# Performance work log

Hardware: AMD Instinct MI355X
Metric: run time of the kernel (lower is better)

The kernel has to match this reference:

```python
import jax, jax.numpy as jnp
import numpy as np


def _binarize(w):
    # adaptive per-output-channel scale: alpha = mean(|w|) over input dim (detached)
    alpha = jax.lax.stop_gradient(jnp.mean(jnp.abs(w), axis=1, keepdims=True))
    bw = alpha * jnp.sign(w)
    # straight-through estimator: forward uses bw, backward passes grad to w
    return w + jax.lax.stop_gradient(bw - w)


def setup_inputs() -> dict:
    key = jax.random.key(0)
    k1, k2, k3, k4, k5 = jax.random.split(key, 5)
    D, H = 1024, 4096
    x = jax.random.normal(k1, (64, 196, D), dtype=jnp.float32)
    w1 = jax.random.normal(k2, (H, D), dtype=jnp.float32) * 0.02
    b1 = jax.random.normal(k3, (H,), dtype=jnp.float32) * 0.02
    w2 = jax.random.normal(k4, (D, H), dtype=jnp.float32) * 0.02
    b2 = jax.random.normal(k5, (D,), dtype=jnp.float32) * 0.02
    return {"x": x, "w1": w1, "b1": b1, "w2": w2, "b2": b2}


def reference(x, w1, b1, w2, b2):
    # fc1: binary-weight linear -> GELU (exact, erf) -> fc2: binary-weight linear
    # dropout prob = 0.0 -> identity
    bw1 = _binarize(w1)  # [H, D]
    h = jnp.einsum('bsd,hd->bsh', x, bw1) + b1  # [B, S, H]
    h = jax.nn.gelu(h, approximate=False)
    bw2 = _binarize(w2)  # [D, H]
    out = jnp.einsum('bsh,dh->bsd', h, bw2) + b2  # [B, S, D]
    return out
```

## Files before the change

kernel.cpp:

```cpp
#include <hip/hip_runtime.h>
#include <hip/hip_bf16.h>
#include <cstdint>
#include <cstddef>

typedef __bf16 bf16x8 __attribute__((ext_vector_type(8)));
typedef float f32x4 __attribute__((ext_vector_type(4)));

#define AS1(p) ((const __attribute__((address_space(1))) void*)(p))
#define AS3(p) ((__attribute__((address_space(3))) void*)(p))
#define LDSA(p) ((unsigned)(size_t)(const __attribute__((address_space(3))) unsigned short*)(p))

__device__ __forceinline__ unsigned short f2bf_rne(float f) {
    union { float f; unsigned u; } c; c.f = f;
    unsigned u = c.u;
    unsigned r = (u + 0x7FFFu + ((u >> 16) & 1u)) >> 16;
    return (unsigned short)r;
}

__global__ __launch_bounds__(256)
void binarize_k(const float* __restrict__ W, unsigned short* __restrict__ Sg,
                float* __restrict__ Alpha, int C) {
    const int r = blockIdx.x;
    const float4* w = (const float4*)(W + (size_t)r * C);
    ushort4* s = (ushort4*)(Sg + (size_t)r * C);
    const int n4 = C >> 2;
    float lsum = 0.f;
    for (int i = threadIdx.x; i < n4; i += 256) {
        float4 v = w[i];
        lsum += fabsf(v.x) + fabsf(v.y) + fabsf(v.z) + fabsf(v.w);
        ushort4 o;
        o.x = (v.x == 0.f) ? 0 : ((v.x < 0.f) ? 0xBF80 : 0x3F80);
        o.y = (v.y == 0.f) ? 0 : ((v.y < 0.f) ? 0xBF80 : 0x3F80);
        o.z = (v.z == 0.f) ? 0 : ((v.z < 0.f) ? 0xBF80 : 0x3F80);
        o.w = (v.w == 0.f) ? 0 : ((v.w < 0.f) ? 0xBF80 : 0x3F80);
        s[i] = o;
    }
    for (int o = 32; o > 0; o >>= 1) lsum += __shfl_down(lsum, o, 64);
    __shared__ float red[4];
    const int lane = threadIdx.x & 63, wid = threadIdx.x >> 6;
    if (lane == 0) red[wid] = lsum;
    __syncthreads();
    if (threadIdx.x == 0) Alpha[r] = (red[0] + red[1] + red[2] + red[3]) / (float)C;
}

__global__ __launch_bounds__(256)
void f32_to_bf16_k(const float* __restrict__ X, unsigned short* __restrict__ Y, int n4) {
    const int stride = gridDim.x * 256;
    for (int i = blockIdx.x * 256 + threadIdx.x; i < n4; i += stride) {
        float4 v = ((const float4*)X)[i];
        ushort4 o;
        o.x = f2bf_rne(v.x); o.y = f2bf_rne(v.y);
        o.z = f2bf_rne(v.z); o.w = f2bf_rne(v.w);
        ((ushort4*)Y)[i] = o;
    }
}

template<int GELU>
__global__ __launch_bounds__(512, 2)
void gemm_bin8(const unsigned short* __restrict__ A,
               const unsigned short* __restrict__ S,
               const float* __restrict__ alpha,
               const float* __restrict__ bias,
               unsigned short* __restrict__ Obf,
               float* __restrict__ Of32,
               int M, int N, int K)
{
    __shared__ __align__(16) unsigned short lds[2][2][2][128 * 64];

    const int tid  = threadIdx.x;
    const int lane = tid & 63;
    const int wid  = tid >> 6;
    const int wr   = wid >> 2;
    const int wc   = wid & 3;
    const int lr   = lane & 15;
    const int hi   = lane >> 4;
    const int xorv = lr & 7;

    const int nbn = N >> 8, nbm = M >> 8;
    const int nwg = nbm * nbn;
    const int q = nwg >> 3, r = nwg & 7;
    const int xcd = blockIdx.x & 7, loc = blockIdx.x >> 3;
    const int swz = (xcd < r ? xcd * (q + 1) : r * (q + 1) + (xcd - r) * q) + loc;
    const int bm = swz / nbn, bn = swz % nbn;

    const unsigned short* gA = A + (size_t)bm * 256 * K;
    const unsigned short* gB = S + (size_t)bn * 256 * K;

    const unsigned short* Ab[2] = { &lds[0][0][wr][0], &lds[1][0][wr][0] };
    const unsigned short* Bb[2] = { &lds[0][1][wc >> 1][0], &lds[1][1][wc >> 1][0] };
    const int brow = (wc & 1) * 64;

    f32x4 acc[8][4] = {};
    bf16x8 af[2][4], bq0[2][2], bq1[2][2];

    const int T = K >> 6;
    const int niter = T >> 1;

#define STAGE(BUF_, MAT_, HALF_, TILE_, GSRC_) do {                                   \
    const unsigned short* _g = (GSRC_) + (size_t)(HALF_) * 128 * K + ((TILE_) << 6);  \
    unsigned short* _l = &lds[BUF_][MAT_][HALF_][0];                                  \
    _Pragma("unroll")                                                                 \
    for (int _rd = 0; _rd < 2; ++_rd) {                                               \
        const int _u = _rd * 512 + tid;                                               \
        const int _row = _u >> 3;                                                     \
        const int _sc = ((_u & 7) ^ (_row & 7)) << 3;                                 \
        __builtin_amdgcn_global_load_lds(AS1(_g + (size_t)_row * K + _sc),            \
                                         AS3(_l + _u * 8), 16, 0, 0);                 \
    }                                                                                 \
} while (0)

#define DSR(DST_, PTR_) do {                                                          \
    f32x4 _t;                                                                         \
    asm volatile("ds_read_b128 %0, %1" : "=v"(_t) : "v"(LDSA(PTR_)));                 \
    DST_ = __builtin_bit_cast(bf16x8, _t);                                            \
} while (0)

#define LOAD_AF(BUF_, MB_) do {                                                       \
    _Pragma("unroll")                                                                 \
    for (int _ks = 0; _ks < 2; ++_ks)                                                 \
    _Pragma("unroll")                                                                 \
    for (int _mf = 0; _mf < 4; ++_mf)                                                 \
        DSR(af[_ks][_mf], Ab[BUF_] + (((MB_)*4 + _mf) * 16 + lr) * 64                 \
                          + (((_ks << 2) + hi) ^ xorv) * 8);                          \
} while (0)

#define LOAD_BF(ARR_, BUF_, NB_) do {                                                 \
    _Pragma("unroll")                                                                 \
    for (int _ks = 0; _ks < 2; ++_ks)                                                 \
    _Pragma("unroll")                                                                 \
    for (int _nf = 0; _nf < 2; ++_nf)                                                 \
        DSR(ARR_[_ks][_nf], Bb[BUF_] + (brow + ((NB_)*2 + _nf) * 16 + lr) * 64        \
                            + (((_ks << 2) + hi) ^ xorv) * 8);                        \
} while (0)

#define MFMA_Q(MB_, ARR_, NB_) do {                                                   \
    _Pragma("unroll")                                                                 \
    for (int _ks = 0; _ks < 2; ++_ks)                                                 \
    _Pragma("unroll")                                                                 \
    for (int _mf = 0; _mf < 4; ++_mf)                                                 \
    _Pragma("unroll")                                                                 \
    for (int _nf = 0; _nf < 2; ++_nf)                                                 \
        acc[(MB_)*4 + _mf][(NB_)*2 + _nf] = __builtin_amdgcn_mfma_f32_16x16x32_bf16(  \
            af[_ks][_mf], ARR_[_ks][_nf], acc[(MB_)*4 + _mf][(NB_)*2 + _nf], 0, 0, 0);\
} while (0)

#define BAR() __builtin_amdgcn_s_barrier()
#define VMW4() asm volatile("s_waitcnt vmcnt(4)" ::: "memory")
#define LGKM0() do {                                                                  \
    asm volatile("s_waitcnt lgkmcnt(0)" ::: "memory");                                \
    __builtin_amdgcn_sched_barrier(0);                                                \
} while (0)
#define MFMA_PHASE(MB_, ARR_, NB_) do {                                               \
    BAR(); LGKM0();                                                                   \
    __builtin_amdgcn_s_setprio(1);                                                    \
    MFMA_Q(MB_, ARR_, NB_);                                                           \
    __builtin_amdgcn_sched_barrier(0);                                                \
    __builtin_amdgcn_s_setprio(0);                                                    \
    BAR();                                                                            \
} while (0)

    STAGE(0, 1, 0, 0, gB); STAGE(0, 1, 1, 0, gB);
    STAGE(0, 0, 0, 0, gA); STAGE(0, 0, 1, 0, gA);
    STAGE(1, 1, 0, 1, gB); STAGE(1, 1, 1, 1, gB);
    VMW4();
    BAR();

    for (int i = 0; i < niter; ++i) {
        const int t  = 2 * i;
        const int t1 = t + 1;
        const int t2 = (t + 2 < T) ? t + 2 : 0;
        const int t3 = (t + 3 < T) ? t + 3 : 1;

        LOAD_AF(0, 0); LOAD_BF(bq0, 0, 0);
        STAGE(1, 0, 0, t1, gA);
        MFMA_PHASE(0, bq0, 0);
        LOAD_BF(bq1, 0, 1);
        STAGE(1, 0, 1, t1, gA);
        MFMA_PHASE(0, bq1, 1);
        LOAD_AF(0, 1);
        STAGE(0, 1, 0, t2, gB);
        MFMA_PHASE(1, bq0, 0);
        STAGE(0, 1, 1, t2, gB);
        BAR(); LGKM0();
        __builtin_amdgcn_s_setprio(1);
        MFMA_Q(1, bq1, 1);
        __builtin_amdgcn_sched_barrier(0);
        __builtin_amdgcn_s_setprio(0);
        VMW4(); BAR();
        LOAD_AF(1, 0); LOAD_BF(bq0, 1, 0);
        STAGE(0, 0, 0, t2, gA);
        MFMA_PHASE(0, bq0, 0);
        LOAD_BF(bq1, 1, 1);
        STAGE(0, 0, 1, t2, gA);
        MFMA_PHASE(0, bq1, 1);
        LOAD_AF(1, 1);
        STAGE(1, 1, 0, t3, gB);
        MFMA_PHASE(1, bq0, 0);
        STAGE(1, 1, 1, t3, gB);
        BAR(); LGKM0();
        __builtin_amdgcn_s_setprio(1);
        MFMA_Q(1, bq1, 1);
        __builtin_amdgcn_sched_barrier(0);
        __builtin_amdgcn_s_setprio(0);
        VMW4(); BAR();
    }

    const int col0 = bn * 256 + wc * 64;
    const int row0 = bm * 256 + wr * 128;
    float al[4], bi[4];
#pragma unroll
    for (int nf = 0; nf < 4; ++nf) {
        const int n = col0 + nf * 16 + lr;
        al[nf] = alpha[n];
        bi[nf] = bias[n];
    }
#pragma unroll
    for (int mf = 0; mf < 8; ++mf) {
#pragma unroll
        for (int j = 0; j < 4; ++j) {
            const int m = row0 + mf * 16 + hi * 4 + j;
#pragma unroll
            for (int nf = 0; nf < 4; ++nf) {
                const int n = col0 + nf * 16 + lr;
                float v = acc[mf][nf][j] * al[nf] + bi[nf];
                if (GELU) {
                    v = 0.5f * v * (1.0f + erff(v * 0.70710678118654752f));
                    Obf[(size_t)m * N + n] = f2bf_rne(v);
                } else {
                    Of32[(size_t)m * N + n] = v;
                }
            }
        }
    }
#undef STAGE
#undef DSR
#undef LOAD_AF
#undef LOAD_BF
#undef MFMA_Q
#undef BAR
#undef VMW4
#undef LGKM0
#undef MFMA_PHASE
}

extern "C" void kernel_launch(void* const* d_in, const int* in_sizes, int n_in,
                              void* d_out, int out_size, void* d_ws, size_t ws_size,
                              hipStream_t stream) {
    const float* x  = (const float*)d_in[0];
    const float* w1 = (const float*)d_in[1];
    const float* b1 = (const float*)d_in[2];
    const float* w2 = (const float*)d_in[3];
    const float* b2 = (const float*)d_in[4];
    float* out = (float*)d_out;

    const int D = 1024, H = 4096;
    const int M = in_sizes[0] / D;

    char* ws = (char*)d_ws;
    size_t off = 0;
    auto alloc = [&](size_t bytes) -> void* {
        void* p = ws + off;
        off = (off + bytes + 255) & ~(size_t)255;
        return p;
    };
    unsigned short* xb = (unsigned short*)alloc((size_t)M * D * 2);
    unsigned short* s1 = (unsigned short*)alloc((size_t)H * D * 2);
    float*          a1 = (float*)alloc((size_t)H * 4);
    unsigned short* s2 = (unsigned short*)alloc((size_t)D * H * 2);
    float*          a2 = (float*)alloc((size_t)D * 4);
    unsigned short* hb = (unsigned short*)alloc((size_t)M * H * 2);

    binarize_k<<<H, 256, 0, stream>>>(w1, s1, a1, D);
    binarize_k<<<D, 256, 0, stream>>>(w2, s2, a2, H);
    f32_to_bf16_k<<<2048, 256, 0, stream>>>(x, xb, (M * D) / 4);

    gemm_bin8<1><<<(M / 256) * (H / 256), 512, 0, stream>>>(xb, s1, a1, b1, hb, nullptr, M, H, D);
    gemm_bin8<0><<<(M / 256) * (D / 256), 512, 0, stream>>>(hb, s2, a2, b2, nullptr, out, M, D, H);
}
```

Before: 398.3 us.

## Use smaller-tile GEMM kernel for second matmul and relax sched barriers

Adds a simpler 128x64-tile GEMM kernel with 256 threads and uses it for the fc2 matmul (M=12544, N=1024, K=4096). With 256x256 tiles that GEMM launched only 196 workgroups, fewer than the CU count, so the smaller tiles are meant to fill the GPU better. Separately, it removes the sched_barrier after each MFMA block in the big kernel, giving the compiler more freedom to interleave instructions. The new kernel is single-buffered with a full barrier every K step and has less reuse per tile, which may cost efficiency.

```diff
diff --git a/kernel.cpp b/kernel.cpp
--- a/kernel.cpp
+++ b/kernel.cpp
@@ -154,7 +154,6 @@
     BAR(); LGKM0();                                                                   \
     __builtin_amdgcn_s_setprio(1);                                                    \
     MFMA_Q(MB_, ARR_, NB_);                                                           \
-    __builtin_amdgcn_sched_barrier(0);                                                \
     __builtin_amdgcn_s_setprio(0);                                                    \
     BAR();                                                                            \
 } while (0)
@@ -174,33 +173,38 @@
         LOAD_AF(0, 0); LOAD_BF(bq0, 0, 0);
         STAGE(1, 0, 0, t1, gA);
         MFMA_PHASE(0, bq0, 0);
+
         LOAD_BF(bq1, 0, 1);
         STAGE(1, 0, 1, t1, gA);
         MFMA_PHASE(0, bq1, 1);
+
         LOAD_AF(0, 1);
         STAGE(0, 1, 0, t2, gB);
         MFMA_PHASE(1, bq0, 0);
+
         STAGE(0, 1, 1, t2, gB);
         BAR(); LGKM0();
         __builtin_amdgcn_s_setprio(1);
         MFMA_Q(1, bq1, 1);
-        __builtin_amdgcn_sched_barrier(0);
         __builtin_amdgcn_s_setprio(0);
         VMW4(); BAR();
+
         LOAD_AF(1, 0); LOAD_BF(bq0, 1, 0);
         STAGE(0, 0, 0, t2, gA);
         MFMA_PHASE(0, bq0, 0);
+
         LOAD_BF(bq1, 1, 1);
         STAGE(0, 0, 1, t2, gA);
         MFMA_PHASE(0, bq1, 1);
+
         LOAD_AF(1, 1);
         STAGE(1, 1, 0, t3, gB);
         MFMA_PHASE(1, bq0, 0);
+
         STAGE(1, 1, 1, t3, gB);
         BAR(); LGKM0();
         __builtin_amdgcn_s_setprio(1);
         MFMA_Q(1, bq1, 1);
-        __builtin_amdgcn_sched_barrier(0);
         __builtin_amdgcn_s_setprio(0);
         VMW4(); BAR();
     }
@@ -241,6 +245,114 @@
 #undef VMW4
 #undef LGKM0
 #undef MFMA_PHASE
+}
+
+template<int GELU, int BN>
+__global__ __launch_bounds__(256)
+void gemm_bin(const unsigned short* __restrict__ A,
+              const unsigned short* __restrict__ S,
+              const float* __restrict__ alpha,
+              const float* __restrict__ bias,
+              unsigned short* __restrict__ Obf,
+              float* __restrict__ Of32,
+              int M, int N, int K)
+{
+    constexpr int WN = BN / 2;
+    constexpr int NFRAG = WN / 16;
+
+    __shared__ __align__(16) unsigned short As[128 * 64];
+    __shared__ __align__(16) unsigned short Ss[BN * 64];
+
+    const int tid  = threadIdx.x;
+    const int lane = tid & 63;
+    const int wid  = tid >> 6;
+    const int wr   = wid >> 1, wc = wid & 1;
+    const int lr   = lane & 15;
+    const int hi   = lane >> 4;
+    const int xorv = lr & 7;
+
+    const int nbn = N / BN, nbm = M >> 7;
+    const int nwg = nbm * nbn;
+    const int q = nwg >> 3, r = nwg & 7;
+    const int xcd = blockIdx.x & 7, loc = blockIdx.x >> 3;
+    const int swz = (xcd < r ? xcd * (q + 1) : r * (q + 1) + (xcd - r) * q) + loc;
+    const int bm = swz / nbn, bn = swz % nbn;
+
+    const unsigned short* gA = A + (size_t)bm * 128 * K;
+    const unsigned short* gS = S + (size_t)bn * BN * K;
+
+    f32x4 acc[4][NFRAG] = {};
+
+    const int nkt = K >> 6;
+    for (int kt = 0; kt < nkt; ++kt) {
+        const int k0 = kt << 6;
+#pragma unroll
+        for (int j = 0; j < 4; ++j) {
+            const int u = j * 256 + tid;
+            const int row = u >> 3;
+            const int sc = ((u & 7) ^ (row & 7)) << 3;
+            __builtin_amdgcn_global_load_lds(AS1(gA + (size_t)row * K + k0 + sc),
+                                             AS3(&As[0] + u * 8), 16, 0, 0);
+        }
+#pragma unroll
+        for (int j = 0; j < BN / 32; ++j) {
+            const int u = j * 256 + tid;
+            const int row = u >> 3;
+            const int sc = ((u & 7) ^ (row & 7)) << 3;
+            __builtin_amdgcn_global_load_lds(AS1(gS + (size_t)row * K + k0 + sc),
+                                             AS3(&Ss[0] + u * 8), 16, 0, 0);
+        }
+        __syncthreads();
+
+        bf16x8 af[2][4], bf[2][NFRAG];
+#pragma unroll
+        for (int ks = 0; ks < 2; ++ks) {
+            const int kg = ((ks << 2) + hi) ^ xorv;
+#pragma unroll
+            for (int mf = 0; mf < 4; ++mf)
+                af[ks][mf] = *(const bf16x8*)(&As[0] + (wr * 64 + mf * 16 + lr) * 64 + kg * 8);
+#pragma unroll
+            for (int nf = 0; nf < NFRAG; ++nf)
+                bf[ks][nf] = *(const bf16x8*)(&Ss[0] + (wc * WN + nf * 16 + lr) * 64 + kg * 8);
+        }
+#pragma unroll
+        for (int ks = 0; ks < 2; ++ks)
+#pragma unroll
+            for (int mf = 0; mf < 4; ++mf)
+#pragma unroll
+                for (int nf = 0; nf < NFRAG; ++nf)
+                    acc[mf][nf] = __builtin_amdgcn_mfma_f32_16x16x32_bf16(
+                        af[ks][mf], bf[ks][nf], acc[mf][nf], 0, 0, 0);
+        __syncthreads();
+    }
+
+    const int col0 = bn * BN + wc * WN;
+    const int row0 = bm * 128 + wr * 64;
+    float al[NFRAG], bi[NFRAG];
+#pragma unroll
+    for (int nf = 0; nf < NFRAG; ++nf) {
+        const int n = col0 + nf * 16 + lr;
+        al[nf] = alpha[n];
+        bi[nf] = bias[n];
+    }
+#pragma unroll
+    for (int mf = 0; mf < 4; ++mf) {
+#pragma unroll
+        for (int j = 0; j < 4; ++j) {
+            const int m = row0 + mf * 16 + hi * 4 + j;
+#pragma unroll
+            for (int nf = 0; nf < NFRAG; ++nf) {
+                const int n = col0 + nf * 16 + lr;
+                float v = acc[mf][nf][j] * al[nf] + bi[nf];
+                if (GELU) {
+                    v = 0.5f * v * (1.0f + erff(v * 0.70710678118654752f));
+                    Obf[(size_t)m * N + n] = f2bf_rne(v);
+                } else {
+                    Of32[(size_t)m * N + n] = v;
+                }
+            }
+        }
+    }
 }
 
 extern "C" void kernel_launch(void* const* d_in, const int* in_sizes, int n_in,
@@ -275,5 +387,5 @@
     f32_to_bf16_k<<<2048, 256, 0, stream>>>(x, xb, (M * D) / 4);
 
     gemm_bin8<1><<<(M / 256) * (H / 256), 512, 0, stream>>>(xb, s1, a1, b1, hb, nullptr, M, H, D);
-    gemm_bin8<0><<<(M / 256) * (D / 256), 512, 0, stream>>>(hb, s2, a2, b2, nullptr, out, M, D, H);
-}
+    gemm_bin<0, 64><<<(M / 128) * (D / 64), 256, 0, stream>>>(hb, s2, a2, b2, nullptr, out, M, D, H);
+}
```

Result: slower. 419.6 us (+5.4%).
